# Performance work log

Measured on AMD Instinct MI355X. Metric: run time of the kernel, lower is better.

## Reference

```python
import jax, jax.numpy as jnp
import numpy as np

B = 1048576
H = 16  # LSTM hidden size

def setup_inputs() -> dict:
    key = jax.random.key(0)
    ks = jax.random.split(key, 16)
    s = 1.0 / np.sqrt(H)
    return {
        "mobility": jax.random.normal(ks[0], (B, 7, 1), dtype=jnp.float32),
        "controls": jax.random.normal(ks[1], (B, 5), dtype=jnp.float32),
        "last": jax.random.normal(ks[2], (B, 1), dtype=jnp.float32),
        # cc: Linear(5 -> 3)
        "W_cc": jax.random.uniform(ks[3], (3, 5), jnp.float32, -s, s),
        "b_cc": jax.random.uniform(ks[4], (3,), jnp.float32, -s, s),
        # LSTM(input=1, hidden=16), gate order i,f,g,o
        "W_ih": jax.random.uniform(ks[5], (4 * H, 1), jnp.float32, -s, s),
        "W_hh": jax.random.uniform(ks[6], (4 * H, H), jnp.float32, -s, s),
        "b_ih": jax.random.uniform(ks[7], (4 * H,), jnp.float32, -s, s),
        "b_hh": jax.random.uniform(ks[8], (4 * H,), jnp.float32, -s, s),
        # fc: Linear(19->16), Tanh, Dropout(eval=identity), Linear(16->16), Tanh, Linear(16->1), ReLU
        "W1": jax.random.uniform(ks[9], (16, 19), jnp.float32, -s, s),
        "b1": jax.random.uniform(ks[10], (16,), jnp.float32, -s, s),
        "W2": jax.random.uniform(ks[11], (16, 16), jnp.float32, -s, s),
        "b2": jax.random.uniform(ks[12], (16,), jnp.float32, -s, s),
        "W3": jax.random.uniform(ks[13], (1, 16), jnp.float32, -s, s),
        "b3": jax.random.uniform(ks[14], (1,), jnp.float32, -s, s),
    }

def _lstm(x, W_ih, W_hh, b_ih, b_hh):
    # x: [B, T, 1] -> final hidden state [B, H]
    b = x.shape[0]
    h0 = jnp.zeros((b, H), x.dtype)
    c0 = jnp.zeros((b, H), x.dtype)
    bias = b_ih + b_hh

    def step(carry, x_t):
        h, c = carry
        gates = x_t @ W_ih.T + h @ W_hh.T + bias  # [B, 4H]
        i, f, g, o = jnp.split(gates, 4, axis=-1)
        i = jax.nn.sigmoid(i)
        f = jax.nn.sigmoid(f)
        g = jnp.tanh(g)
        o = jax.nn.sigmoid(o)
        c = f * c + i * g
        h = o * jnp.tanh(c)
        return (h, c), None

    (h, c), _ = jax.lax.scan(step, (h0, c0), jnp.swapaxes(x, 0, 1))
    return h

def reference(mobility, controls, last, W_cc, b_cc, W_ih, W_hh, b_ih, b_hh, W1, b1, W2, b2, W3, b3):
    control = controls @ W_cc.T + b_cc                 # [B, 3]
    m = _lstm(mobility, W_ih, W_hh, b_ih, b_hh)        # [B, 16] final hidden
    x = jnp.concatenate([m, control], axis=1)          # [B, 19]
    x = jnp.tanh(x @ W1.T + b1)                        # dropout is identity (eval)
    x = jnp.tanh(x @ W2.T + b2)
    out = jax.nn.relu(x @ W3.T + b3)                   # [B, 1]
    return out
```

## Files before the change

### kernel.cpp

```cpp
#include <hip/hip_runtime.h>
#include <hip/hip_bf16.h>

typedef _Float16 f16x8  __attribute__((ext_vector_type(8)));
typedef _Float16 f16x16 __attribute__((ext_vector_type(16)));
typedef float    f32x16 __attribute__((ext_vector_type(16)));
typedef float    v2f    __attribute__((ext_vector_type(2)));
typedef unsigned u32x4  __attribute__((ext_vector_type(4)));

#define LOG2E 1.442695040888963f

__device__ __forceinline__ unsigned pk16(float a, float b) {
    return __builtin_bit_cast(unsigned, __builtin_amdgcn_cvt_pkrtz(a, b));
}

__global__ __launch_bounds__(256, 3) void lstm_mfma_kernel(
    const float* __restrict__ mobility,
    const float* __restrict__ controls,
    const float* __restrict__ W_cc, const float* __restrict__ b_cc,
    const float* __restrict__ W_ih, const float* __restrict__ W_hh,
    const float* __restrict__ b_ih, const float* __restrict__ b_hh,
    const float* __restrict__ W1,  const float* __restrict__ b1,
    const float* __restrict__ W2,  const float* __restrict__ b2,
    const float* __restrict__ W3,  const float* __restrict__ b3,
    float* __restrict__ out, int Btot)
{
    __shared__ float hbuf[256][17];

    const int tid  = threadIdx.x;
    const int lane = tid & 63;
    const int wib  = tid >> 6;
    const int col  = lane & 31;
    const int hi   = lane >> 5;

    const int blockRow0 = blockIdx.x * 256;
    const int r_lo = blockRow0 + wib * 64 + col;
    const int r_hi = r_lo + 32;

    float mlo[7], mhi[7];
    #pragma unroll
    for (int t = 0; t < 7; ++t) { mlo[t] = mobility[r_lo * 7 + t]; mhi[t] = mobility[r_hi * 7 + t]; }

    f16x8 afrag[2];
    #pragma unroll
    for (int gb = 0; gb < 2; ++gb) {
        const float s = (gb == 0) ? -LOG2E : ((col < 16) ? 2.0f * LOG2E : -LOG2E);
        const float* wr = W_hh + (gb * 32 + col) * 16 + hi * 8;
        u32x4 aw = { pk16(s * wr[0], s * wr[1]), pk16(s * wr[2], s * wr[3]),
                     pk16(s * wr[4], s * wr[5]), pk16(s * wr[6], s * wr[7]) };
        afrag[gb] = __builtin_bit_cast(f16x8, aw);
    }

    f16x16 bias_h[2], wih_h[2];
    #pragma unroll
    for (int gb = 0; gb < 2; ++gb)
        #pragma unroll
        for (int q = 0; q < 4; ++q) {
            const int gu = gb * 32 + 8 * q + 4 * hi;
            const float s = (gu < 32) ? -LOG2E : ((gu < 48) ? 2.0f * LOG2E : -LOG2E);
            #pragma unroll
            for (int e = 0; e < 4; ++e) {
                bias_h[gb][4 * q + e] = (_Float16)(s * (b_ih[gu + e] + b_hh[gu + e]));
                wih_h [gb][4 * q + e] = (_Float16)(s * W_ih[gu + e]);
            }
        }

    float c[2][8];
    #pragma unroll
    for (int rb = 0; rb < 2; ++rb)
        #pragma unroll
        for (int u = 0; u < 8; ++u) c[rb][u] = 0.0f;

    u32x4 bz = { 0u, 0u, 0u, 0u };
    f16x8 bfrag[2];
    bfrag[0] = __builtin_bit_cast(f16x8, bz);
    bfrag[1] = __builtin_bit_cast(f16x8, bz);

    #pragma unroll 1
    for (int t = 0; t < 7; ++t) {
        #pragma unroll
        for (int rb = 0; rb < 2; ++rb) {
            const float xt = rb ? mhi[t] : mlo[t];

            f32x16 cin0, cin1;
            #pragma unroll
            for (int r = 0; r < 16; ++r)
                cin0[r] = fmaf(xt, (float)wih_h[0][r], (float)bias_h[0][r]);
            f32x16 a0 = __builtin_amdgcn_mfma_f32_32x32x16_f16(afrag[0], bfrag[rb], cin0, 0, 0, 0);
            #pragma unroll
            for (int r = 0; r < 16; ++r)
                cin1[r] = fmaf(xt, (float)wih_h[1][r], (float)bias_h[1][r]);
            f32x16 a1 = __builtin_amdgcn_mfma_f32_32x32x16_f16(afrag[1], bfrag[rb], cin1, 0, 0, 0);

            float dh[8], nh[8], h[8];
            #pragma unroll
            for (int u = 0; u < 8; ++u) {
                const float ea = __builtin_amdgcn_exp2f(a0[u]);
                const float ef = __builtin_amdgcn_exp2f(a0[u + 8]);
                const float eb = __builtin_amdgcn_exp2f(a1[u]);
                const float eo = __builtin_amdgcn_exp2f(a1[u + 8]);
                const float pf   = 1.0f + ef;
                const float pa   = 1.0f + ea;
                const float den1 = fmaf(pa, eb, pa);
                const float D    = den1 * pf;
                const float rD   = __builtin_amdgcn_rcpf(D);
                const float num  = fmaf(eb, 2.0f * LOG2E, -2.0f * LOG2E);
                const float m1   = num * pf;
                const float cn   = fmaf(c[rb][u], den1, m1);
                const float cs   = cn * rD;
                c[rb][u] = cs;
                const float ec   = __builtin_amdgcn_exp2f(cs);
                const float ph   = 1.0f + eo;
                dh[u] = fmaf(ph, ec, ph);
                nh[u] = ec - 1.0f;
            }
            #pragma unroll
            for (int u = 0; u < 8; u += 2) {
                const float P  = dh[u] * dh[u + 1];
                const float rP = __builtin_amdgcn_rcpf(P);
                h[u]     = (nh[u]     * dh[u + 1]) * rP;
                h[u + 1] = (nh[u + 1] * dh[u])     * rP;
            }
            unsigned q0 = pk16(h[0], h[1]);
            unsigned q1 = pk16(h[2], h[3]);
            unsigned q2 = pk16(h[4], h[5]);
            unsigned q3 = pk16(h[6], h[7]);
            auto s02 = __builtin_amdgcn_permlane32_swap(q0, q2, false, false);
            auto s13 = __builtin_amdgcn_permlane32_swap(q1, q3, false, false);
            u32x4 bw = { s02[0], s13[0], s02[1], s13[1] };
            bfrag[rb] = __builtin_bit_cast(f16x8, bw);
        }
    }

    #pragma unroll
    for (int rb = 0; rb < 2; ++rb) {
        const int rr = wib * 64 + col + rb * 32;
        #pragma unroll
        for (int e = 0; e < 8; ++e)
            hbuf[rr][hi * 8 + e] = (float)bfrag[rb][e];
    }
    __syncthreads();

    const int grow = blockRow0 + tid;

    float x19[19];
    #pragma unroll
    for (int k = 0; k < 16; ++k) x19[k] = hbuf[tid][k];

    float ctl[5];
    #pragma unroll
    for (int k = 0; k < 5; ++k) ctl[k] = controls[grow * 5 + k];
    #pragma unroll
    for (int j = 0; j < 3; ++j) {
        float a = b_cc[j];
        #pragma unroll
        for (int k = 0; k < 5; ++k) a = fmaf(ctl[k], W_cc[j * 5 + k], a);
        x19[16 + j] = a;
    }

    float d1[16];
    #pragma unroll
    for (int j = 0; j < 16; ++j) {
        float a = b1[j];
        #pragma unroll
        for (int k = 0; k < 19; ++k) a = fmaf(x19[k], W1[j * 19 + k], a);
        d1[j] = __builtin_amdgcn_exp2f((2.0f * LOG2E) * a) + 1.0f;
    }
    v2f t12[8];
    #pragma unroll
    for (int j = 0; j < 16; j += 2) {
        const float rP = __builtin_amdgcn_rcpf(d1[j] * d1[j + 1]);
        t12[j >> 1][0] = fmaf(-2.0f * d1[j + 1], rP, 1.0f);
        t12[j >> 1][1] = fmaf(-2.0f * d1[j],     rP, 1.0f);
    }

    float d2[16];
    #pragma unroll
    for (int j = 0; j < 16; ++j) {
        const v2f* w2row = (const v2f*)(W2 + j * 16);
        v2f a = t12[0] * w2row[0];
        #pragma unroll
        for (int p = 1; p < 8; ++p) a = __builtin_elementwise_fma(t12[p], w2row[p], a);
        d2[j] = __builtin_amdgcn_exp2f((2.0f * LOG2E) * (a.x + a.y + b2[j])) + 1.0f;
    }
    v2f t22[8];
    #pragma unroll
    for (int j = 0; j < 16; j += 2) {
        const float rP = __builtin_amdgcn_rcpf(d2[j] * d2[j + 1]);
        t22[j >> 1][0] = fmaf(-2.0f * d2[j + 1], rP, 1.0f);
        t22[j >> 1][1] = fmaf(-2.0f * d2[j],     rP, 1.0f);
    }

    const v2f* w3p = (const v2f*)W3;
    v2f a3 = t22[0] * w3p[0];
    #pragma unroll
    for (int p = 1; p < 8; ++p) a3 = __builtin_elementwise_fma(t22[p], w3p[p], a3);
    const float r = a3.x + a3.y + b3[0];
    if (grow < Btot) out[grow] = fmaxf(r, 0.0f);
}

extern "C" void kernel_launch(void* const* d_in, const int* in_sizes, int n_in,
                              void* d_out, int out_size, void* d_ws, size_t ws_size,
                              hipStream_t stream) {
    const float* mobility = (const float*)d_in[0];
    const float* controls = (const float*)d_in[1];
    const float* W_cc = (const float*)d_in[3];
    const float* b_cc = (const float*)d_in[4];
    const float* W_ih = (const float*)d_in[5];
    const float* W_hh = (const float*)d_in[6];
    const float* b_ih = (const float*)d_in[7];
    const float* b_hh = (const float*)d_in[8];
    const float* W1   = (const float*)d_in[9];
    const float* b1   = (const float*)d_in[10];
    const float* W2   = (const float*)d_in[11];
    const float* b2   = (const float*)d_in[12];
    const float* W3   = (const float*)d_in[13];
    const float* b3   = (const float*)d_in[14];
    float* out = (float*)d_out;

    const int Btot = in_sizes[0] / 7;
    const int grid = (Btot + 255) / 256;

    lstm_mfma_kernel<<<grid, 256, 0, stream>>>(
        mobility, controls, W_cc, b_cc, W_ih, W_hh, b_ih, b_hh,
        W1, b1, W2, b2, W3, b3, out, Btot);
}
```

Baseline: 115.4 us.

## Stage mobility via coalesced LDS loads and pair cell-state reciprocals

Mobility rows are now loaded cooperatively per wave into shared memory with coalesced accesses, replacing strided per-lane global loads, and each timestep reads its input from LDS. The cell-state update now shares one reciprocal across two units, removing half of those rcp operations at the cost of extra multiplies. A sched_barrier is added after each row-block step to constrain instruction scheduling. The risks are extra LDS traffic inside the recurrence, possible overflow in the paired product D0*D1, and a missing sync between the LDS writes and reads (probably safe because each wave reads only its own rows).

```diff
diff --git a/kernel.cpp b/kernel.cpp
--- a/kernel.cpp
+++ b/kernel.cpp
@@ -25,6 +25,7 @@
     float* __restrict__ out, int Btot)
 {
     __shared__ float hbuf[256][17];
+    __shared__ float mobs[256][7];
 
     const int tid  = threadIdx.x;
     const int lane = tid & 63;
@@ -33,12 +34,13 @@
     const int hi   = lane >> 5;
 
     const int blockRow0 = blockIdx.x * 256;
-    const int r_lo = blockRow0 + wib * 64 + col;
-    const int r_hi = r_lo + 32;
-
-    float mlo[7], mhi[7];
-    #pragma unroll
-    for (int t = 0; t < 7; ++t) { mlo[t] = mobility[r_lo * 7 + t]; mhi[t] = mobility[r_hi * 7 + t]; }
+
+    {
+        float* dst = &mobs[wib * 64][0];
+        const float* src = mobility + (size_t)(blockRow0 + wib * 64) * 7;
+        #pragma unroll
+        for (int j = 0; j < 7; ++j) dst[lane + j * 64] = src[lane + j * 64];
+    }
 
     f16x8 afrag[2];
     #pragma unroll
@@ -79,7 +81,7 @@
     for (int t = 0; t < 7; ++t) {
         #pragma unroll
         for (int rb = 0; rb < 2; ++rb) {
-            const float xt = rb ? mhi[t] : mlo[t];
+            const float xt = mobs[wib * 64 + col + rb * 32][t];
 
             f32x16 cin0, cin1;
             #pragma unroll
@@ -91,34 +93,40 @@
                 cin1[r] = fmaf(xt, (float)wih_h[1][r], (float)bias_h[1][r]);
             f32x16 a1 = __builtin_amdgcn_mfma_f32_32x32x16_f16(afrag[1], bfrag[rb], cin1, 0, 0, 0);
 
-            float dh[8], nh[8], h[8];
-            #pragma unroll
-            for (int u = 0; u < 8; ++u) {
-                const float ea = __builtin_amdgcn_exp2f(a0[u]);
-                const float ef = __builtin_amdgcn_exp2f(a0[u + 8]);
-                const float eb = __builtin_amdgcn_exp2f(a1[u]);
-                const float eo = __builtin_amdgcn_exp2f(a1[u + 8]);
-                const float pf   = 1.0f + ef;
-                const float pa   = 1.0f + ea;
-                const float den1 = fmaf(pa, eb, pa);
-                const float D    = den1 * pf;
-                const float rD   = __builtin_amdgcn_rcpf(D);
-                const float num  = fmaf(eb, 2.0f * LOG2E, -2.0f * LOG2E);
-                const float m1   = num * pf;
-                const float cn   = fmaf(c[rb][u], den1, m1);
-                const float cs   = cn * rD;
-                c[rb][u] = cs;
-                const float ec   = __builtin_amdgcn_exp2f(cs);
-                const float ph   = 1.0f + eo;
-                dh[u] = fmaf(ph, ec, ph);
-                nh[u] = ec - 1.0f;
-            }
+            float h[8];
             #pragma unroll
             for (int u = 0; u < 8; u += 2) {
-                const float P  = dh[u] * dh[u + 1];
-                const float rP = __builtin_amdgcn_rcpf(P);
-                h[u]     = (nh[u]     * dh[u + 1]) * rP;
-                h[u + 1] = (nh[u + 1] * dh[u])     * rP;
+                const float ea0 = __builtin_amdgcn_exp2f(a0[u]);
+                const float ef0 = __builtin_amdgcn_exp2f(a0[u + 8]);
+                const float eb0 = __builtin_amdgcn_exp2f(a1[u]);
+                const float eo0 = __builtin_amdgcn_exp2f(a1[u + 8]);
+                const float ea1 = __builtin_amdgcn_exp2f(a0[u + 1]);
+                const float ef1 = __builtin_amdgcn_exp2f(a0[u + 9]);
+                const float eb1 = __builtin_amdgcn_exp2f(a1[u + 1]);
+                const float eo1 = __builtin_amdgcn_exp2f(a1[u + 9]);
+
+                const float pf0 = 1.0f + ef0, pa0 = 1.0f + ea0;
+                const float pf1 = 1.0f + ef1, pa1 = 1.0f + ea1;
+                const float den0 = fmaf(pa0, eb0, pa0);
+                const float den1 = fmaf(pa1, eb1, pa1);
+                const float D0 = den0 * pf0, D1 = den1 * pf1;
+                const float num0 = fmaf(eb0, 2.0f * LOG2E, -2.0f * LOG2E);
+                const float num1 = fmaf(eb1, 2.0f * LOG2E, -2.0f * LOG2E);
+                const float cn0 = fmaf(c[rb][u],     den0, num0 * pf0);
+                const float cn1 = fmaf(c[rb][u + 1], den1, num1 * pf1);
+                const float rC = __builtin_amdgcn_rcpf(D0 * D1);
+                const float cs0 = (cn0 * D1) * rC;
+                const float cs1 = (cn1 * D0) * rC;
+                c[rb][u]     = cs0;
+                c[rb][u + 1] = cs1;
+                const float ec0 = __builtin_amdgcn_exp2f(cs0);
+                const float ec1 = __builtin_amdgcn_exp2f(cs1);
+                const float ph0 = 1.0f + eo0, ph1 = 1.0f + eo1;
+                const float dh0 = fmaf(ph0, ec0, ph0);
+                const float dh1 = fmaf(ph1, ec1, ph1);
+                const float rP = __builtin_amdgcn_rcpf(dh0 * dh1);
+                h[u]     = ((ec0 - 1.0f) * dh1) * rP;
+                h[u + 1] = ((ec1 - 1.0f) * dh0) * rP;
             }
             unsigned q0 = pk16(h[0], h[1]);
             unsigned q1 = pk16(h[2], h[3]);
@@ -128,6 +136,8 @@
             auto s13 = __builtin_amdgcn_permlane32_swap(q1, q3, false, false);
             u32x4 bw = { s02[0], s13[0], s02[1], s13[1] };
             bfrag[rb] = __builtin_bit_cast(f16x8, bw);
+
+            __builtin_amdgcn_sched_barrier(0);
         }
     }
 
```

After: 117.8 us. 1.02x slower.

## Use persistent grid-stride blocks and pair cell-state reciprocals in LSTM loop

Applied to the files above, without the earlier changes.

Turns the kernel into a persistent one: the grid is capped at 1024 blocks and each block loops over 256-row tiles. The per-block setup of weight fragments, bias and W_ih conversions then happens once per block instead of once per tile. The LSTM gate math is regrouped into pairs of units with v2f operations, sharing one reciprocal between two cell-state divisions and cutting rcp instructions. The trade-offs are an extra barrier per tile, possible load imbalance across the capped grid, and slightly different rounding from the shared reciprocal.

```diff
diff --git a/kernel.cpp b/kernel.cpp
--- a/kernel.cpp
+++ b/kernel.cpp
@@ -12,6 +12,7 @@
 __device__ __forceinline__ unsigned pk16(float a, float b) {
     return __builtin_bit_cast(unsigned, __builtin_amdgcn_cvt_pkrtz(a, b));
 }
+__device__ __forceinline__ float fexp2(float x) { return __builtin_amdgcn_exp2f(x); }
 
 __global__ __launch_bounds__(256, 3) void lstm_mfma_kernel(
     const float* __restrict__ mobility,
@@ -32,14 +33,6 @@
     const int col  = lane & 31;
     const int hi   = lane >> 5;
 
-    const int blockRow0 = blockIdx.x * 256;
-    const int r_lo = blockRow0 + wib * 64 + col;
-    const int r_hi = r_lo + 32;
-
-    float mlo[7], mhi[7];
-    #pragma unroll
-    for (int t = 0; t < 7; ++t) { mlo[t] = mobility[r_lo * 7 + t]; mhi[t] = mobility[r_hi * 7 + t]; }
-
     f16x8 afrag[2];
     #pragma unroll
     for (int gb = 0; gb < 2; ++gb) {
@@ -49,7 +42,6 @@
                      pk16(s * wr[4], s * wr[5]), pk16(s * wr[6], s * wr[7]) };
         afrag[gb] = __builtin_bit_cast(f16x8, aw);
     }
-
     f16x16 bias_h[2], wih_h[2];
     #pragma unroll
     for (int gb = 0; gb < 2; ++gb)
@@ -64,138 +56,157 @@
             }
         }
 
-    float c[2][8];
-    #pragma unroll
-    for (int rb = 0; rb < 2; ++rb)
-        #pragma unroll
-        for (int u = 0; u < 8; ++u) c[rb][u] = 0.0f;
-
-    u32x4 bz = { 0u, 0u, 0u, 0u };
-    f16x8 bfrag[2];
-    bfrag[0] = __builtin_bit_cast(f16x8, bz);
-    bfrag[1] = __builtin_bit_cast(f16x8, bz);
-
-    #pragma unroll 1
-    for (int t = 0; t < 7; ++t) {
+    const v2f one   = { 1.0f, 1.0f };
+    const v2f twoL  = { 2.0f * LOG2E, 2.0f * LOG2E };
+    const v2f ntwoL = { -2.0f * LOG2E, -2.0f * LOG2E };
+
+    const int tilesTotal = (Btot + 255) >> 8;
+    for (int tile = blockIdx.x; tile < tilesTotal; tile += gridDim.x) {
+        const int blockRow0 = tile * 256;
+        const int r_lo = blockRow0 + wib * 64 + col;
+        const int r_hi = r_lo + 32;
+
+        float mlo[7], mhi[7];
+        #pragma unroll
+        for (int t = 0; t < 7; ++t) { mlo[t] = mobility[(size_t)r_lo * 7 + t]; mhi[t] = mobility[(size_t)r_hi * 7 + t]; }
+
+        float c[2][8];
+        #pragma unroll
+        for (int rb = 0; rb < 2; ++rb)
+            #pragma unroll
+            for (int u = 0; u < 8; ++u) c[rb][u] = 0.0f;
+
+        u32x4 bz = { 0u, 0u, 0u, 0u };
+        f16x8 bfrag[2];
+        bfrag[0] = __builtin_bit_cast(f16x8, bz);
+        bfrag[1] = __builtin_bit_cast(f16x8, bz);
+
+        #pragma unroll 1
+        for (int t = 0; t < 7; ++t) {
+            #pragma unroll
+            for (int rb = 0; rb < 2; ++rb) {
+                const float xt = rb ? mhi[t] : mlo[t];
+
+                f32x16 cin0, cin1;
+                #pragma unroll
+                for (int r = 0; r < 16; ++r)
+                    cin0[r] = fmaf(xt, (float)wih_h[0][r], (float)bias_h[0][r]);
+                f32x16 a0 = __builtin_amdgcn_mfma_f32_32x32x16_f16(afrag[0], bfrag[rb], cin0, 0, 0, 0);
+                #pragma unroll
+                for (int r = 0; r < 16; ++r)
+                    cin1[r] = fmaf(xt, (float)wih_h[1][r], (float)bias_h[1][r]);
+                f32x16 a1 = __builtin_amdgcn_mfma_f32_32x32x16_f16(afrag[1], bfrag[rb], cin1, 0, 0, 0);
+
+                float h[8];
+                #pragma unroll
+                for (int u = 0; u < 8; u += 2) {
+                    v2f ea = { fexp2(a0[u]),     fexp2(a0[u + 1]) };
+                    v2f ef = { fexp2(a0[u + 8]), fexp2(a0[u + 9]) };
+                    v2f eb = { fexp2(a1[u]),     fexp2(a1[u + 1]) };
+                    v2f eo = { fexp2(a1[u + 8]), fexp2(a1[u + 9]) };
+                    v2f pf  = one + ef;
+                    v2f pa  = one + ea;
+                    v2f den = __builtin_elementwise_fma(pa, eb, pa);
+                    v2f D   = den * pf;
+                    v2f num = __builtin_elementwise_fma(eb, twoL, ntwoL);
+                    v2f cv  = { c[rb][u], c[rb][u + 1] };
+                    v2f cn  = __builtin_elementwise_fma(cv, den, num * pf);
+                    const float rC = __builtin_amdgcn_rcpf(D[0] * D[1]);
+                    v2f Dsw = { D[1], D[0] };
+                    v2f rCv = { rC, rC };
+                    v2f cs  = (cn * Dsw) * rCv;
+                    c[rb][u]     = cs[0];
+                    c[rb][u + 1] = cs[1];
+                    v2f ec = { fexp2(cs[0]), fexp2(cs[1]) };
+                    v2f ph = one + eo;
+                    v2f dh = __builtin_elementwise_fma(ph, ec, ph);
+                    v2f nh = ec - one;
+                    const float rP = __builtin_amdgcn_rcpf(dh[0] * dh[1]);
+                    v2f dsw = { dh[1], dh[0] };
+                    v2f rPv = { rP, rP };
+                    v2f hv  = (nh * dsw) * rPv;
+                    h[u]     = hv[0];
+                    h[u + 1] = hv[1];
+                }
+                unsigned q0 = pk16(h[0], h[1]);
+                unsigned q1 = pk16(h[2], h[3]);
+                unsigned q2 = pk16(h[4], h[5]);
+                unsigned q3 = pk16(h[6], h[7]);
+                auto s02 = __builtin_amdgcn_permlane32_swap(q0, q2, false, false);
+                auto s13 = __builtin_amdgcn_permlane32_swap(q1, q3, false, false);
+                u32x4 bw = { s02[0], s13[0], s02[1], s13[1] };
+                bfrag[rb] = __builtin_bit_cast(f16x8, bw);
+            }
+        }
+
         #pragma unroll
         for (int rb = 0; rb < 2; ++rb) {
-            const float xt = rb ? mhi[t] : mlo[t];
-
-            f32x16 cin0, cin1;
-            #pragma unroll
-            for (int r = 0; r < 16; ++r)
-                cin0[r] = fmaf(xt, (float)wih_h[0][r], (float)bias_h[0][r]);
-            f32x16 a0 = __builtin_amdgcn_mfma_f32_32x32x16_f16(afrag[0], bfrag[rb], cin0, 0, 0, 0);
-            #pragma unroll
-            for (int r = 0; r < 16; ++r)
-                cin1[r] = fmaf(xt, (float)wih_h[1][r], (float)bias_h[1][r]);
-            f32x16 a1 = __builtin_amdgcn_mfma_f32_32x32x16_f16(afrag[1], bfrag[rb], cin1, 0, 0, 0);
-
-            float dh[8], nh[8], h[8];
-            #pragma unroll
-            for (int u = 0; u < 8; ++u) {
-                const float ea = __builtin_amdgcn_exp2f(a0[u]);
-                const float ef = __builtin_amdgcn_exp2f(a0[u + 8]);
-                const float eb = __builtin_amdgcn_exp2f(a1[u]);
-                const float eo = __builtin_amdgcn_exp2f(a1[u + 8]);
-                const float pf   = 1.0f + ef;
-                const float pa   = 1.0f + ea;
-                const float den1 = fmaf(pa, eb, pa);
-                const float D    = den1 * pf;
-                const float rD   = __builtin_amdgcn_rcpf(D);
-                const float num  = fmaf(eb, 2.0f * LOG2E, -2.0f * LOG2E);
-                const float m1   = num * pf;
-                const float cn   = fmaf(c[rb][u], den1, m1);
-                const float cs   = cn * rD;
-                c[rb][u] = cs;
-                const float ec   = __builtin_amdgcn_exp2f(cs);
-                const float ph   = 1.0f + eo;
-                dh[u] = fmaf(ph, ec, ph);
-                nh[u] = ec - 1.0f;
-            }
-            #pragma unroll
-            for (int u = 0; u < 8; u += 2) {
-                const float P  = dh[u] * dh[u + 1];
-                const float rP = __builtin_amdgcn_rcpf(P);
-                h[u]     = (nh[u]     * dh[u + 1]) * rP;
-                h[u + 1] = (nh[u + 1] * dh[u])     * rP;
-            }
-            unsigned q0 = pk16(h[0], h[1]);
-            unsigned q1 = pk16(h[2], h[3]);
-            unsigned q2 = pk16(h[4], h[5]);
-            unsigned q3 = pk16(h[6], h[7]);
-            auto s02 = __builtin_amdgcn_permlane32_swap(q0, q2, false, false);
-            auto s13 = __builtin_amdgcn_permlane32_swap(q1, q3, false, false);
-            u32x4 bw = { s02[0], s13[0], s02[1], s13[1] };
-            bfrag[rb] = __builtin_bit_cast(f16x8, bw);
-        }
+            const int rr = wib * 64 + col + rb * 32;
+            #pragma unroll
+            for (int e = 0; e < 8; ++e)
+                hbuf[rr][hi * 8 + e] = (float)bfrag[rb][e];
+        }
+        __syncthreads();
+
+        const int grow = blockRow0 + tid;
+
+        float x19[19];
+        #pragma unroll
+        for (int k = 0; k < 16; ++k) x19[k] = hbuf[tid][k];
+
+        float ctl[5];
+        #pragma unroll
+        for (int k = 0; k < 5; ++k) ctl[k] = controls[(size_t)grow * 5 + k];
+        #pragma unroll
+        for (int j = 0; j < 3; ++j) {
+            float a = b_cc[j];
+            #pragma unroll
+            for (int k = 0; k < 5; ++k) a = fmaf(ctl[k], W_cc[j * 5 + k], a);
+            x19[16 + j] = a;
+        }
+
+        float d1[16];
+        #pragma unroll
+        for (int j = 0; j < 16; ++j) {
+            float a = b1[j];
+            #pragma unroll
+            for (int k = 0; k < 19; ++k) a = fmaf(x19[k], W1[j * 19 + k], a);
+            d1[j] = fexp2((2.0f * LOG2E) * a) + 1.0f;
+        }
+        v2f t12[8];
+        #pragma unroll
+        for (int j = 0; j < 16; j += 2) {
+            const float rP = __builtin_amdgcn_rcpf(d1[j] * d1[j + 1]);
+            t12[j >> 1][0] = fmaf(-2.0f * d1[j + 1], rP, 1.0f);
+            t12[j >> 1][1] = fmaf(-2.0f * d1[j],     rP, 1.0f);
+        }
+
+        float d2[16];
+        #pragma unroll
+        for (int j = 0; j < 16; ++j) {
+            const v2f* w2row = (const v2f*)(W2 + j * 16);
+            v2f a = t12[0] * w2row[0];
+            #pragma unroll
+            for (int p = 1; p < 8; ++p) a = __builtin_elementwise_fma(t12[p], w2row[p], a);
+            d2[j] = fexp2((2.0f * LOG2E) * (a.x + a.y + b2[j])) + 1.0f;
+        }
+        v2f t22[8];
+        #pragma unroll
+        for (int j = 0; j < 16; j += 2) {
+            const float rP = __builtin_amdgcn_rcpf(d2[j] * d2[j + 1]);
+            t22[j >> 1][0] = fmaf(-2.0f * d2[j + 1], rP, 1.0f);
+            t22[j >> 1][1] = fmaf(-2.0f * d2[j],     rP, 1.0f);
+        }
+
+        const v2f* w3p = (const v2f*)W3;
+        v2f a3 = t22[0] * w3p[0];
+        #pragma unroll
+        for (int p = 1; p < 8; ++p) a3 = __builtin_elementwise_fma(t22[p], w3p[p], a3);
+        const float r = a3.x + a3.y + b3[0];
+        if (grow < Btot) out[grow] = fmaxf(r, 0.0f);
+
+        __syncthreads();
     }
-
-    #pragma unroll
-    for (int rb = 0; rb < 2; ++rb) {
-        const int rr = wib * 64 + col + rb * 32;
-        #pragma unroll
-        for (int e = 0; e < 8; ++e)
-            hbuf[rr][hi * 8 + e] = (float)bfrag[rb][e];
-    }
-    __syncthreads();
-
-    const int grow = blockRow0 + tid;
-
-    float x19[19];
-    #pragma unroll
-    for (int k = 0; k < 16; ++k) x19[k] = hbuf[tid][k];
-
-    float ctl[5];
-    #pragma unroll
-    for (int k = 0; k < 5; ++k) ctl[k] = controls[grow * 5 + k];
-    #pragma unroll
-    for (int j = 0; j < 3; ++j) {
-        float a = b_cc[j];
-        #pragma unroll
-        for (int k = 0; k < 5; ++k) a = fmaf(ctl[k], W_cc[j * 5 + k], a);
-        x19[16 + j] = a;
-    }
-
-    float d1[16];
-    #pragma unroll
-    for (int j = 0; j < 16; ++j) {
-        float a = b1[j];
-        #pragma unroll
-        for (int k = 0; k < 19; ++k) a = fmaf(x19[k], W1[j * 19 + k], a);
-        d1[j] = __builtin_amdgcn_exp2f((2.0f * LOG2E) * a) + 1.0f;
-    }
-    v2f t12[8];
-    #pragma unroll
-    for (int j = 0; j < 16; j += 2) {
-        const float rP = __builtin_amdgcn_rcpf(d1[j] * d1[j + 1]);
-        t12[j >> 1][0] = fmaf(-2.0f * d1[j + 1], rP, 1.0f);
-        t12[j >> 1][1] = fmaf(-2.0f * d1[j],     rP, 1.0f);
-    }
-
-    float d2[16];
-    #pragma unroll
-    for (int j = 0; j < 16; ++j) {
-        const v2f* w2row = (const v2f*)(W2 + j * 16);
-        v2f a = t12[0] * w2row[0];
-        #pragma unroll
-        for (int p = 1; p < 8; ++p) a = __builtin_elementwise_fma(t12[p], w2row[p], a);
-        d2[j] = __builtin_amdgcn_exp2f((2.0f * LOG2E) * (a.x + a.y + b2[j])) + 1.0f;
-    }
-    v2f t22[8];
-    #pragma unroll
-    for (int j = 0; j < 16; j += 2) {
-        const float rP = __builtin_amdgcn_rcpf(d2[j] * d2[j + 1]);
-        t22[j >> 1][0] = fmaf(-2.0f * d2[j + 1], rP, 1.0f);
-        t22[j >> 1][1] = fmaf(-2.0f * d2[j],     rP, 1.0f);
-    }
-
-    const v2f* w3p = (const v2f*)W3;
-    v2f a3 = t22[0] * w3p[0];
-    #pragma unroll
-    for (int p = 1; p < 8; ++p) a3 = __builtin_elementwise_fma(t22[p], w3p[p], a3);
-    const float r = a3.x + a3.y + b3[0];
-    if (grow < Btot) out[grow] = fmaxf(r, 0.0f);
 }
 
 extern "C" void kernel_launch(void* const* d_in, const int* in_sizes, int n_in,
@@ -217,8 +228,9 @@
     const float* b3   = (const float*)d_in[14];
     float* out = (float*)d_out;
 
-    const int Btot = in_sizes[0] / 7;
-    const int grid = (Btot + 255) / 256;
+    const int Btot  = in_sizes[0] / 7;
+    const int tiles = (Btot + 255) / 256;
+    const int grid  = tiles < 1024 ? tiles : 1024;
 
     lstm_mfma_kernel<<<grid, 256, 0, stream>>>(
         mobility, controls, W_cc, b_cc, W_ih, W_hh, b_ih, b_hh,
```

Result: no change. 113.9 us (-1.3%).
